# Performance work log

Hardware: AMD Instinct MI355X
Metric: run time of the kernel (lower is better)

Reference implementation:

```python
import jax, jax.numpy as jnp
import numpy as np
from jax import lax

V, E, T, F, K = 100000, 300, 50, 100, 3
B, S = 32, 512


def setup_inputs() -> dict:
    key = jax.random.key(0)
    ks = jax.random.split(key, 10)
    inp = {
        "x": jax.random.randint(ks[0], (B, S), 0, V),
        "tags": jax.random.randint(ks[1], (B, S), 0, T),
        "emb": jax.random.normal(ks[2], (V, E), dtype=jnp.float32),
        "conv_w": jax.random.normal(ks[3], (F, E, K), dtype=jnp.float32) / np.sqrt(E * K),
        "conv_b": jnp.zeros((F,), dtype=jnp.float32),
        "fc_w": jax.random.normal(ks[4], (T, F), dtype=jnp.float32) / np.sqrt(F),
        "fc_b": jnp.zeros((T,), dtype=jnp.float32),
        "start_trans": jax.random.uniform(ks[5], (T,), dtype=jnp.float32, minval=-0.1, maxval=0.1),
        "end_trans": jax.random.uniform(ks[6], (T,), dtype=jnp.float32, minval=-0.1, maxval=0.1),
        "trans": jax.random.uniform(ks[7], (T, T), dtype=jnp.float32, minval=-0.1, maxval=0.1),
    }
    return inp


def _emissions(x, emb, conv_w, conv_b, fc_w, fc_b):
    e = emb[x]                                   # [B,S,E] embedding gather
    e = jnp.transpose(e, (0, 2, 1))              # [B,E,S]
    h = lax.conv_general_dilated(e, conv_w, (1,), [(K // 2, K // 2)])  # [B,F,S] (NCW/OIW)
    h = jax.nn.relu(h + conv_b[None, :, None])   # dropout is identity in eval
    feat = jnp.transpose(h, (0, 2, 1))           # [B,S,F]
    return (jnp.einsum("bsf,tf->bst", feat, fc_w) + fc_b).astype(jnp.float32)  # [B,S,T]


def _crf_nll(emissions, tags, start_trans, end_trans, trans):
    # numerator: score of the gold tag path (full mask)
    em_tag = jnp.take_along_axis(emissions, tags[..., None], axis=-1)[..., 0]  # [B,S]
    num = (start_trans[tags[:, 0]]
           + em_tag.sum(-1)
           + trans[tags[:, :-1], tags[:, 1:]].sum(-1)
           + end_trans[tags[:, -1]])                                           # [B]

    # denominator: forward algorithm via scan over time
    alpha0 = start_trans[None, :] + emissions[:, 0]                             # [B,T]

    def step(alpha, em_t):
        # alpha: [B,T] prev scores; em_t: [B,T] emissions at t
        new = jax.nn.logsumexp(alpha[:, :, None] + trans[None] + em_t[:, None, :], axis=1)
        return new, None

    alpha, _ = lax.scan(step, alpha0, jnp.transpose(emissions[:, 1:], (1, 0, 2)))
    log_z = jax.nn.logsumexp(alpha + end_trans[None, :], axis=-1)               # [B]
    return -(num - log_z).sum()  # torchcrf default reduction='sum'; model returns -llh


def reference(x, tags, emb, conv_w, conv_b, fc_w, fc_b, start_trans, end_trans, trans):
    emissions = _emissions(x, emb, conv_w, conv_b, fc_w, fc_b)
    return _crf_nll(emissions, tags, start_trans, end_trans, trans)
```

## Files before the change

### kernel.cpp

```cpp
#include <hip/hip_runtime.h>
#include <hip/hip_bf16.h>
#include <math.h>

#define BB 32
#define SS 512
#define EE 300
#define FF 100
#define TT 50
#define CH 16
#define NC 32

typedef __attribute__((ext_vector_type(8))) short v8s;
typedef __attribute__((ext_vector_type(4))) float v4f;
#define MFMA16 __builtin_amdgcn_mfma_f32_16x16x32_bf16

#define AP 328
#define NCH 10
#define CKS 3
#define CHB (128 * 96)
#define A2P 152
#define MP 72

__device__ inline unsigned short f2bf(float v) {
    unsigned u = __float_as_uint(v);
    unsigned r = u + 0x7fff + ((u >> 16) & 1);
    return (unsigned short)(r >> 16);
}
__device__ inline float bf2f(short s) {
    return __uint_as_float(((unsigned)(unsigned short)s) << 16);
}
__device__ inline v8s ldsld8(const short* p) {
    return *(const v8s*)__builtin_assume_aligned(p, 16);
}
__device__ inline void g2lds16(const void* g, void* l) {
    __builtin_amdgcn_global_load_lds(
        (const __attribute__((address_space(1))) unsigned int*)g,
        (__attribute__((address_space(3))) unsigned int*)l, 16, 0, 0);
}

__global__ void prep_kernel(const float* __restrict__ tr, const float* __restrict__ cw,
                            const float* __restrict__ fcw,
                            unsigned short* __restrict__ wB2,
                            unsigned short* __restrict__ fcwT2,
                            unsigned short* __restrict__ AT,
                            unsigned short* __restrict__ Ab)
{
    const int gid = blockIdx.x * 256 + threadIdx.x;
    const int gs  = 64 * 256;
    for (int idx = gid; idx < NCH * CKS * 8 * 512; idx += gs) {
        int e = idx & 7, p = (idx >> 3) & 63, blk = idx >> 9;
        int ch = blk / 24, rem = blk - ch * 24;
        int sl = rem >> 3, ft = rem & 7;
        int col = p >> 2, q = p & 3;
        int n  = ft * 16 + col;
        int gk = ch * 96 + sl * 32 + q * 8 + e;
        int kk = gk / 320, ee = gk - kk * 320;
        float v = (n < FF && ee < EE) ? cw[n * 900 + ee * 3 + kk] : 0.f;
        wB2[idx] = f2bf(v);
    }
    for (int idx = gid; idx < 16 * 512; idx += gs) {
        int e = idx & 7, p = (idx >> 3) & 63, blk = idx >> 9;
        int ks = blk >> 2, nt = blk & 3;
        int col = p >> 2, q = p & 3;
        int t = nt * 16 + col, f = ks * 32 + q * 8 + e;
        float v = (t < TT && f < FF) ? fcw[t * FF + f] : 0.f;
        fcwT2[idx] = f2bf(v);
    }
    for (int idx = gid; idx < 64 * 64; idx += gs) {
        int r = idx >> 6, c2 = idx & 63;
        AT[idx] = (r < TT && c2 < TT) ? f2bf(__expf(tr[c2 * TT + r])) : 0;
        Ab[idx] = (r < TT && c2 < TT) ? f2bf(__expf(tr[r * TT + c2])) : 0;
    }
}

__global__ __launch_bounds__(256, 2) void emis_kernel(
    const int* __restrict__ x, const float* __restrict__ emb,
    const unsigned short* __restrict__ wB2, const float* __restrict__ cb,
    const unsigned short* __restrict__ fcwT2, const float* __restrict__ fcb,
    const int* __restrict__ tags,
    float* __restrict__ expem, float* __restrict__ rmv, float* __restrict__ emtag)
{
    __shared__ __align__(16) short ldsA[34 * AP];
    __shared__ __align__(16) short ldsB[2][CHB];

    const int b    = blockIdx.y;
    const int s0   = blockIdx.x * 32;
    const int tid  = threadIdx.x;
    const int wv   = tid >> 6;
    const int lane = tid & 63;
    const int col  = lane & 15;
    const int q    = lane >> 4;
    const int bofs = ((col << 2) | q) << 3;

#pragma unroll
    for (int it = 0; it < 6; ++it) {
        int seg = it * 4 + wv;
        g2lds16((const char*)wB2 + seg * 1024 + lane * 16,
                (char*)ldsB[0] + seg * 1024);
    }

    for (int g = tid; g < 34 * 75; g += 256) {
        int r = g / 75, eg = g - r * 75; int e0 = eg * 4;
        int gsq = s0 - 1 + r;
        short4 o;
        if (gsq >= 0 && gsq < SS) {
            int xr = x[b * SS + gsq];
            const float4 v = *(const float4*)(emb + (size_t)xr * EE + e0);
            o = make_short4((short)f2bf(v.x), (short)f2bf(v.y),
                            (short)f2bf(v.z), (short)f2bf(v.w));
        } else o = make_short4(0, 0, 0, 0);
        *(short4*)&ldsA[r * AP + e0] = o;
    }
    if (tid < 34 * 5) {
        int r = tid / 5, c0 = 300 + (tid % 5) * 4;
        *(short4*)&ldsA[r * AP + c0] = make_short4(0, 0, 0, 0);
    }
    __syncthreads();

    v4f acc[2][2];
#pragma unroll
    for (int a = 0; a < 2; ++a)
#pragma unroll
        for (int f = 0; f < 2; ++f) acc[a][f] = (v4f){0.f, 0.f, 0.f, 0.f};

    const int ftA = wv * 2, ftB = wv * 2 + 1;
    for (int ch = 0; ch < NCH; ++ch) {
        if (ch < NCH - 1) {
            const char* g = (const char*)(wB2 + (size_t)(ch + 1) * CHB);
            char* l = (char*)ldsB[(ch + 1) & 1];
#pragma unroll
            for (int it = 0; it < 6; ++it) {
                int seg = it * 4 + wv;
                g2lds16(g + seg * 1024 + lane * 16, l + seg * 1024);
            }
        }
        const short* Bc = ldsB[ch & 1];
#pragma unroll
        for (int sl = 0; sl < CKS; ++sl) {
            int gk = ch * 96 + sl * 32;
            int kk = (gk >= 640) ? 2 : (gk >= 320 ? 1 : 0);
            int e0 = gk - kk * 320;
            v8s a0 = ldsld8(&ldsA[(col + kk) * AP + e0 + q * 8]);
            v8s a1 = ldsld8(&ldsA[(16 + col + kk) * AP + e0 + q * 8]);
            v8s b0 = ldsld8(&Bc[((sl * 8 + ftA) << 9) + bofs]);
            v8s b1 = ldsld8(&Bc[((sl * 8 + ftB) << 9) + bofs]);
            acc[0][0] = MFMA16(a0, b0, acc[0][0], 0, 0, 0);
            acc[0][1] = MFMA16(a0, b1, acc[0][1], 0, 0, 0);
            acc[1][0] = MFMA16(a1, b0, acc[1][0], 0, 0, 0);
            acc[1][1] = MFMA16(a1, b1, acc[1][1], 0, 0, 0);
        }
        __syncthreads();
    }

    short* A2 = ldsB[0];
    short* B2 = ldsB[1];
#pragma unroll
    for (int it = 0; it < 4; ++it) {
        int seg = it * 4 + wv;
        g2lds16((const char*)fcwT2 + seg * 1024 + lane * 16,
                (char*)B2 + seg * 1024);
    }
#pragma unroll
    for (int st = 0; st < 2; ++st)
#pragma unroll
        for (int fi = 0; fi < 2; ++fi) {
            int f = (wv * 2 + fi) * 16 + col;
            float bias = (f < FF) ? cb[f] : 0.f;
#pragma unroll
            for (int rg = 0; rg < 4; ++rg) {
                int s = st * 16 + q * 4 + rg;
                float v = (f < FF) ? fmaxf(acc[st][fi][rg] + bias, 0.f) : 0.f;
                A2[s * A2P + f] = (short)f2bf(v);
            }
        }
    __syncthreads();

    if (wv < 2) {
        v4f a2[4];
#pragma unroll
        for (int nt = 0; nt < 4; ++nt) a2[nt] = (v4f){0.f, 0.f, 0.f, 0.f};
#pragma unroll
        for (int ks = 0; ks < 4; ++ks) {
            v8s af = ldsld8(&A2[(wv * 16 + col) * A2P + ks * 32 + q * 8]);
#pragma unroll
            for (int nt = 0; nt < 4; ++nt) {
                v8s bt = ldsld8(&B2[((ks * 4 + nt) << 9) + bofs]);
                a2[nt] = MFMA16(af, bt, a2[nt], 0, 0, 0);
            }
        }
        float fb0 = fcb[col], fb1 = fcb[16 + col], fb2 = fcb[32 + col];
        float fb3 = (col < 2) ? fcb[48 + col] : 0.f;
#pragma unroll
        for (int rg = 0; rg < 4; ++rg) {
            int s = s0 + wv * 16 + q * 4 + rg;
            float e0v = a2[0][rg] + fb0;
            float e1v = a2[1][rg] + fb1;
            float e2v = a2[2][rg] + fb2;
            float e3v = (col < 2) ? a2[3][rg] + fb3 : -1e30f;
            float m = fmaxf(fmaxf(e0v, e1v), fmaxf(e2v, e3v));
#pragma unroll
            for (int off = 1; off < 16; off <<= 1) m = fmaxf(m, __shfl_xor(m, off));
            int gidx = b * SS + s;
            if (col == 0) rmv[gidx] = m;
            int tg = tags[gidx];
            float* orow = expem + (size_t)gidx * TT;
            orow[col]      = __expf(e0v - m);
            orow[16 + col] = __expf(e1v - m);
            orow[32 + col] = __expf(e2v - m);
            if (col < 2) orow[48 + col] = __expf(e3v - m);
            if (tg == col)            emtag[gidx] = e0v;
            else if (tg == 16 + col)  emtag[gidx] = e1v;
            else if (tg == 32 + col)  emtag[gidx] = e2v;
            else if (col < 2 && tg == 48 + col) emtag[gidx] = e3v;
        }
    }
}

__global__ __launch_bounds__(64) void chunk_kernel(
    const float* __restrict__ expem, const unsigned short* __restrict__ AT,
    const unsigned short* __restrict__ Ab,
    unsigned short* __restrict__ R, float* __restrict__ lsR)
{
    __shared__ __align__(16) short L[2][64 * MP];
    __shared__ __align__(16) float emL[CH][64];
    const int c = blockIdx.x, b = blockIdx.y;
    const int lane = threadIdx.x;
    const int col = lane & 15, q = lane >> 4;
    const int t0 = c * CH + 1;
    const int nf = (c == NC - 1) ? (SS - 1 - (NC - 1) * CH) : CH;

    for (int idx = lane; idx < CH * 64; idx += 64) {
        int k = idx >> 6, m = idx & 63;
        float v = 0.f;
        if (m < TT && k < nf) v = expem[((size_t)(b * SS + t0 + k)) * TT + m];
        emL[k][m] = v;
    }

    v8s af[4][2];
#pragma unroll
    for (int jt = 0; jt < 4; ++jt)
#pragma unroll
        for (int kc = 0; kc < 2; ++kc)
            af[jt][kc] = *(const v8s*)(AT + (jt * 16 + col) * 64 + kc * 32 + q * 8);
    __syncthreads();

    {
        const v8s* arow = (const v8s*)(Ab + lane * 64);
#pragma unroll
        for (int g = 0; g < 8; ++g) {
            v8s a = arow[g];
            v8s o;
#pragma unroll
            for (int e = 0; e < 8; ++e)
                o[e] = (short)f2bf(bf2f(a[e]) * emL[0][g * 8 + e]);
            *(v8s*)&L[0][lane * MP + g * 8] = o;
        }
    }

    int cur = 0;
    for (int k = 1; k < nf; ++k) {
        __syncthreads();
        v8s bf[4][2];
#pragma unroll
        for (int nt = 0; nt < 4; ++nt)
#pragma unroll
            for (int kc = 0; kc < 2; ++kc)
                bf[nt][kc] = ldsld8(&L[cur][(nt * 16 + col) * MP + kc * 32 + q * 8]);
        v4f acc[4][4];
#pragma unroll
        for (int jt = 0; jt < 4; ++jt)
#pragma unroll
            for (int nt = 0; nt < 4; ++nt) {
                acc[jt][nt] = (v4f){0.f, 0.f, 0.f, 0.f};
                acc[jt][nt] = MFMA16(af[jt][0], bf[nt][0], acc[jt][nt], 0, 0, 0);
                acc[jt][nt] = MFMA16(af[jt][1], bf[nt][1], acc[jt][nt], 0, 0, 0);
            }
        if (k < nf - 1) {
#pragma unroll
            for (int jt = 0; jt < 4; ++jt) {
                const float4 em4 = *(const float4*)&emL[k][jt * 16 + q * 4];
#pragma unroll
                for (int nt = 0; nt < 4; ++nt) {
                    short4 o;
                    o.x = (short)f2bf(acc[jt][nt][0] * em4.x);
                    o.y = (short)f2bf(acc[jt][nt][1] * em4.y);
                    o.z = (short)f2bf(acc[jt][nt][2] * em4.z);
                    o.w = (short)f2bf(acc[jt][nt][3] * em4.w);
                    *(short4*)&L[cur ^ 1][(nt * 16 + col) * MP + jt * 16 + q * 4] = o;
                }
            }
            cur ^= 1;
        } else {
            float vals[4][4][4];
            float mx = 0.f;
#pragma unroll
            for (int jt = 0; jt < 4; ++jt) {
                const float4 em4 = *(const float4*)&emL[k][jt * 16 + q * 4];
#pragma unroll
                for (int nt = 0; nt < 4; ++nt) {
                    vals[jt][nt][0] = acc[jt][nt][0] * em4.x;
                    vals[jt][nt][1] = acc[jt][nt][1] * em4.y;
                    vals[jt][nt][2] = acc[jt][nt][2] * em4.z;
                    vals[jt][nt][3] = acc[jt][nt][3] * em4.w;
#pragma unroll
                    for (int r = 0; r < 4; ++r) mx = fmaxf(mx, vals[jt][nt][r]);
                }
            }
#pragma unroll
            for (int off = 1; off < 64; off <<= 1) mx = fmaxf(mx, __shfl_xor(mx, off));
            mx = fmaxf(mx, 1e-37f);
            float inv = 1.f / mx;
            unsigned short* Rc = R + ((size_t)(b * NC + c) << 12);
#pragma unroll
            for (int jt = 0; jt < 4; ++jt)
#pragma unroll
                for (int nt = 0; nt < 4; ++nt)
#pragma unroll
                    for (int r = 0; r < 4; ++r)
                        Rc[(jt * 16 + q * 4 + r) * 64 + nt * 16 + col] =
                            f2bf(vals[jt][nt][r] * inv);
            if (lane == 0) lsR[b * NC + c] = __logf(mx);
        }
    }
}

__global__ __launch_bounds__(256) void chain_kernel(
    const float* __restrict__ expem, const unsigned short* __restrict__ R,
    const float* __restrict__ lsR, const float* __restrict__ start,
    const float* __restrict__ endt,
    const float* __restrict__ emtag, const float* __restrict__ rmv,
    const int* __restrict__ tags, const float* __restrict__ tr,
    float* __restrict__ nllpart)
{
    __shared__ __align__(16) float pvec[64];
    __shared__ float red[8];
    __shared__ float lzsh;
    const int b = blockIdx.x, tid = threadIdx.x;
    const int wv = tid >> 6, i = tid & 63;

    if (wv == 0) {
        pvec[i] = (i < TT) ? __expf(start[i]) * expem[((size_t)(b * SS)) * TT + i] : 0.f;
        const unsigned short* Rb = R + ((size_t)(b * NC) << 12);
        v8s rb[3][8];
#pragma unroll
        for (int pc = 0; pc < 3; ++pc)
#pragma unroll
            for (int g = 0; g < 8; ++g)
                rb[pc][g] = *(const v8s*)(Rb + ((size_t)pc << 12) + i * 64 + g * 8);
        float logacc = 0.f;
#pragma unroll
        for (int c = 0; c < NC; ++c) {
            const int slot = c % 3;
            float acc = 0.f;
            const float4* pv = (const float4*)pvec;
#pragma unroll
            for (int g = 0; g < 8; ++g) {
                v8s v = rb[slot][g];
                float4 pA = pv[g * 2], pB = pv[g * 2 + 1];
                acc = fmaf(bf2f(v[0]), pA.x, acc);
                acc = fmaf(bf2f(v[1]), pA.y, acc);
                acc = fmaf(bf2f(v[2]), pA.z, acc);
                acc = fmaf(bf2f(v[3]), pA.w, acc);
                acc = fmaf(bf2f(v[4]), pB.x, acc);
                acc = fmaf(bf2f(v[5]), pB.y, acc);
                acc = fmaf(bf2f(v[6]), pB.z, acc);
                acc = fmaf(bf2f(v[7]), pB.w, acc);
            }
            if (c + 3 < NC) {
                const unsigned short* Rn = Rb + ((size_t)(c + 3) << 12);
#pragma unroll
                for (int g = 0; g < 8; ++g)
                    rb[slot][g] = *(const v8s*)(Rn + i * 64 + g * 8);
            }
            float mx = acc;
#pragma unroll
            for (int off = 1; off < 64; off <<= 1) mx = fmaxf(mx, __shfl_xor(mx, off));
            mx = fmaxf(mx, 1e-37f);
            logacc += __logf(mx) + lsR[b * NC + c];
            pvec[i] = acc * (1.f / mx);
        }
        float sv = (i < TT) ? pvec[i] * __expf(endt[i]) : 0.f;
#pragma unroll
        for (int off = 1; off < 64; off <<= 1) sv += __shfl_xor(sv, off);
        if (i == 0) lzsh = logacc + __logf(sv);
    } else {
        float accN = 0.f, accR = 0.f;
        for (int s = tid - 64; s < SS; s += 192) {
            int gi = b * SS + s;
            accN += emtag[gi];
            accR += rmv[gi];
            int tg = tags[gi];
            if (s < SS - 1) accN += tr[tg * TT + tags[gi + 1]];
        }
#pragma unroll
        for (int off = 1; off < 64; off <<= 1) {
            accN += __shfl_xor(accN, off);
            accR += __shfl_xor(accR, off);
        }
        if (i == 0) { red[wv] = accN; red[4 + wv] = accR; }
    }
    __syncthreads();
    if (tid == 0) {
        float tn  = red[1] + red[2] + red[3];
        float trm = red[5] + red[6] + red[7];
        float num = tn + start[tags[b * SS]] + endt[tags[b * SS + SS - 1]];
        nllpart[b] = trm + lzsh - num;
    }
}

__global__ void final_kernel(const float* __restrict__ nllpart, float* __restrict__ out)
{
    int tid = threadIdx.x;
    float v = (tid < BB) ? nllpart[tid] : 0.f;
#pragma unroll
    for (int off = 1; off < 64; off <<= 1) v += __shfl_xor(v, off);
    if (tid == 0) out[0] = v;
}

extern "C" void kernel_launch(void* const* d_in, const int* in_sizes, int n_in,
                              void* d_out, int out_size, void* d_ws, size_t ws_size,
                              hipStream_t stream)
{
    const int*   x    = (const int*)d_in[0];
    const int*   tags = (const int*)d_in[1];
    const float* emb  = (const float*)d_in[2];
    const float* cw   = (const float*)d_in[3];
    const float* cb   = (const float*)d_in[4];
    const float* fcw  = (const float*)d_in[5];
    const float* fcb  = (const float*)d_in[6];
    const float* st   = (const float*)d_in[7];
    const float* en   = (const float*)d_in[8];
    const float* tr   = (const float*)d_in[9];

    unsigned short* wB2   = (unsigned short*)d_ws;
    unsigned short* fcwT2 = wB2 + NCH * CKS * 8 * 512;
    unsigned short* ATm   = fcwT2 + 16 * 512;
    unsigned short* Abm   = ATm + 4096;
    unsigned short* Rm    = Abm + 4096;
    float* fbase   = (float*)(Rm + (size_t)BB * NC * 4096);
    float* expem   = fbase;
    float* rmv     = expem + (size_t)BB * SS * TT;
    float* emtag   = rmv + BB * SS;
    float* lsR     = emtag + BB * SS;
    float* nllpart = lsR + BB * NC;

    prep_kernel<<<dim3(64), 256, 0, stream>>>(tr, cw, fcw, wB2, fcwT2, ATm, Abm);
    emis_kernel<<<dim3(16, BB), 256, 0, stream>>>(x, emb, wB2, cb, fcwT2, fcb,
                                                  tags, expem, rmv, emtag);
    chunk_kernel<<<dim3(NC, BB), 64, 0, stream>>>(expem, ATm, Abm, Rm, lsR);
    chain_kernel<<<dim3(BB), 256, 0, stream>>>(expem, Rm, lsR, st, en,
                                               emtag, rmv, tags, tr, nllpart);
    final_kernel<<<dim3(1), 64, 0, stream>>>(nllpart, (float*)d_out);
}
```

Measured before the change: 249.8 us.

## Single-buffer conv weights, batch embedding gathers, pack bf16, fuse final reduction

The emission kernel drops the double-buffered weight LDS tile to a single buffer and raises the launch bound to three blocks per CU. It reuses ldsA for the FC stage, shrinks its pitch, and issues all embedding gathers up front so more loads are in flight. bf16 conversions use packed two-wide intrinsics. The final reduction kernel is removed: the chain kernel accumulates with atomics and the last block writes the output. The trade-off is that the next weight chunk load no longer overlaps compute, and the float atomic sum order becomes nondeterministic.

```diff
diff --git a/kernel.cpp b/kernel.cpp
--- a/kernel.cpp
+++ b/kernel.cpp
@@ -18,7 +18,7 @@
 #define NCH 10
 #define CKS 3
 #define CHB (128 * 96)
-#define A2P 152
+#define A2P 136
 #define MP 72
 
 __device__ inline unsigned short f2bf(float v) {
@@ -28,6 +28,10 @@
 }
 __device__ inline float bf2f(short s) {
     return __uint_as_float(((unsigned)(unsigned short)s) << 16);
+}
+__device__ inline unsigned pkbf2(float a, float b) {
+    __hip_bfloat162 h = __float22bfloat162_rn(make_float2(a, b));
+    return *(unsigned*)&h;
 }
 __device__ inline v8s ldsld8(const short* p) {
     return *(const v8s*)__builtin_assume_aligned(p, 16);
@@ -43,10 +47,12 @@
                             unsigned short* __restrict__ wB2,
                             unsigned short* __restrict__ fcwT2,
                             unsigned short* __restrict__ AT,
-                            unsigned short* __restrict__ Ab)
+                            unsigned short* __restrict__ Ab,
+                            float* __restrict__ accum, unsigned* __restrict__ cnt)
 {
     const int gid = blockIdx.x * 256 + threadIdx.x;
     const int gs  = 64 * 256;
+    if (gid == 0) { *accum = 0.f; *cnt = 0u; }
     for (int idx = gid; idx < NCH * CKS * 8 * 512; idx += gs) {
         int e = idx & 7, p = (idx >> 3) & 63, blk = idx >> 9;
         int ch = blk / 24, rem = blk - ch * 24;
@@ -73,7 +79,7 @@
     }
 }
 
-__global__ __launch_bounds__(256, 2) void emis_kernel(
+__global__ __launch_bounds__(256, 3) void emis_kernel(
     const int* __restrict__ x, const float* __restrict__ emb,
     const unsigned short* __restrict__ wB2, const float* __restrict__ cb,
     const unsigned short* __restrict__ fcwT2, const float* __restrict__ fcb,
@@ -81,7 +87,7 @@
     float* __restrict__ expem, float* __restrict__ rmv, float* __restrict__ emtag)
 {
     __shared__ __align__(16) short ldsA[34 * AP];
-    __shared__ __align__(16) short ldsB[2][CHB];
+    __shared__ __align__(16) short ldsB[CHB];
 
     const int b    = blockIdx.y;
     const int s0   = blockIdx.x * 32;
@@ -96,26 +102,40 @@
     for (int it = 0; it < 6; ++it) {
         int seg = it * 4 + wv;
         g2lds16((const char*)wB2 + seg * 1024 + lane * 16,
-                (char*)ldsB[0] + seg * 1024);
-    }
-
-    for (int g = tid; g < 34 * 75; g += 256) {
-        int r = g / 75, eg = g - r * 75; int e0 = eg * 4;
-        int gsq = s0 - 1 + r;
-        short4 o;
-        if (gsq >= 0 && gsq < SS) {
-            int xr = x[b * SS + gsq];
-            const float4 v = *(const float4*)(emb + (size_t)xr * EE + e0);
-            o = make_short4((short)f2bf(v.x), (short)f2bf(v.y),
-                            (short)f2bf(v.z), (short)f2bf(v.w));
-        } else o = make_short4(0, 0, 0, 0);
-        *(short4*)&ldsA[r * AP + e0] = o;
+                (char*)ldsB + seg * 1024);
+    }
+
+    int   xr[10], ofs[10], e0a[10];
+#pragma unroll
+    for (int it = 0; it < 10; ++it) {
+        int g = tid + it * 256;
+        int r = g / 75, eg = g - r * 75;
+        int e0 = eg * 4;
+        int src = s0 - 1 + r;
+        bool v = (g < 2550) && (src >= 0) && (src < SS);
+        xr[it]  = v ? x[b * SS + src] : -1;
+        ofs[it] = r * AP + e0;
+        e0a[it] = e0;
+    }
+    float4 vv[10];
+#pragma unroll
+    for (int it = 0; it < 10; ++it)
+        vv[it] = (xr[it] >= 0)
+               ? *(const float4*)(emb + (size_t)xr[it] * EE + e0a[it])
+               : make_float4(0.f, 0.f, 0.f, 0.f);
+#pragma unroll
+    for (int it = 0; it < 10; ++it) {
+        int g = tid + it * 256;
+        if (g < 2550) {
+            unsigned lo = pkbf2(vv[it].x, vv[it].y);
+            unsigned hi = pkbf2(vv[it].z, vv[it].w);
+            *(uint2*)&ldsA[ofs[it]] = make_uint2(lo, hi);
+        }
     }
     if (tid < 34 * 5) {
         int r = tid / 5, c0 = 300 + (tid % 5) * 4;
         *(short4*)&ldsA[r * AP + c0] = make_short4(0, 0, 0, 0);
     }
-    __syncthreads();
 
     v4f acc[2][2];
 #pragma unroll
@@ -125,16 +145,7 @@
 
     const int ftA = wv * 2, ftB = wv * 2 + 1;
     for (int ch = 0; ch < NCH; ++ch) {
-        if (ch < NCH - 1) {
-            const char* g = (const char*)(wB2 + (size_t)(ch + 1) * CHB);
-            char* l = (char*)ldsB[(ch + 1) & 1];
-#pragma unroll
-            for (int it = 0; it < 6; ++it) {
-                int seg = it * 4 + wv;
-                g2lds16(g + seg * 1024 + lane * 16, l + seg * 1024);
-            }
-        }
-        const short* Bc = ldsB[ch & 1];
+        __syncthreads();
 #pragma unroll
         for (int sl = 0; sl < CKS; ++sl) {
             int gk = ch * 96 + sl * 32;
@@ -142,18 +153,26 @@
             int e0 = gk - kk * 320;
             v8s a0 = ldsld8(&ldsA[(col + kk) * AP + e0 + q * 8]);
             v8s a1 = ldsld8(&ldsA[(16 + col + kk) * AP + e0 + q * 8]);
-            v8s b0 = ldsld8(&Bc[((sl * 8 + ftA) << 9) + bofs]);
-            v8s b1 = ldsld8(&Bc[((sl * 8 + ftB) << 9) + bofs]);
+            v8s b0 = ldsld8(&ldsB[((sl * 8 + ftA) << 9) + bofs]);
+            v8s b1 = ldsld8(&ldsB[((sl * 8 + ftB) << 9) + bofs]);
             acc[0][0] = MFMA16(a0, b0, acc[0][0], 0, 0, 0);
             acc[0][1] = MFMA16(a0, b1, acc[0][1], 0, 0, 0);
             acc[1][0] = MFMA16(a1, b0, acc[1][0], 0, 0, 0);
             acc[1][1] = MFMA16(a1, b1, acc[1][1], 0, 0, 0);
         }
         __syncthreads();
-    }
-
-    short* A2 = ldsB[0];
-    short* B2 = ldsB[1];
+        if (ch < NCH - 1) {
+            const char* g = (const char*)(wB2 + (size_t)(ch + 1) * CHB);
+#pragma unroll
+            for (int it = 0; it < 6; ++it) {
+                int seg = it * 4 + wv;
+                g2lds16(g + seg * 1024 + lane * 16, (char*)ldsB + seg * 1024);
+            }
+        }
+    }
+
+    short* A2 = ldsA;
+    short* B2 = ldsB;
 #pragma unroll
     for (int it = 0; it < 4; ++it) {
         int seg = it * 4 + wv;
@@ -249,11 +268,12 @@
 #pragma unroll
         for (int g = 0; g < 8; ++g) {
             v8s a = arow[g];
-            v8s o;
-#pragma unroll
-            for (int e = 0; e < 8; ++e)
-                o[e] = (short)f2bf(bf2f(a[e]) * emL[0][g * 8 + e]);
-            *(v8s*)&L[0][lane * MP + g * 8] = o;
+            float f[8];
+#pragma unroll
+            for (int e = 0; e < 8; ++e) f[e] = bf2f(a[e]) * emL[0][g * 8 + e];
+            uint4 o = make_uint4(pkbf2(f[0], f[1]), pkbf2(f[2], f[3]),
+                                 pkbf2(f[4], f[5]), pkbf2(f[6], f[7]));
+            *(uint4*)&L[0][lane * MP + g * 8] = o;
         }
     }
 
@@ -281,12 +301,10 @@
                 const float4 em4 = *(const float4*)&emL[k][jt * 16 + q * 4];
 #pragma unroll
                 for (int nt = 0; nt < 4; ++nt) {
-                    short4 o;
-                    o.x = (short)f2bf(acc[jt][nt][0] * em4.x);
-                    o.y = (short)f2bf(acc[jt][nt][1] * em4.y);
-                    o.z = (short)f2bf(acc[jt][nt][2] * em4.z);
-                    o.w = (short)f2bf(acc[jt][nt][3] * em4.w);
-                    *(short4*)&L[cur ^ 1][(nt * 16 + col) * MP + jt * 16 + q * 4] = o;
+                    uint2 o = make_uint2(
+                        pkbf2(acc[jt][nt][0] * em4.x, acc[jt][nt][1] * em4.y),
+                        pkbf2(acc[jt][nt][2] * em4.z, acc[jt][nt][3] * em4.w));
+                    *(uint2*)&L[cur ^ 1][(nt * 16 + col) * MP + jt * 16 + q * 4] = o;
                 }
             }
             cur ^= 1;
@@ -330,7 +348,8 @@
     const float* __restrict__ endt,
     const float* __restrict__ emtag, const float* __restrict__ rmv,
     const int* __restrict__ tags, const float* __restrict__ tr,
-    float* __restrict__ nllpart)
+    float* __restrict__ accum, unsigned* __restrict__ cnt,
+    float* __restrict__ out)
 {
     __shared__ __align__(16) float pvec[64];
     __shared__ float red[8];
@@ -404,17 +423,12 @@
         float tn  = red[1] + red[2] + red[3];
         float trm = red[5] + red[6] + red[7];
         float num = tn + start[tags[b * SS]] + endt[tags[b * SS + SS - 1]];
-        nllpart[b] = trm + lzsh - num;
-    }
-}
-
-__global__ void final_kernel(const float* __restrict__ nllpart, float* __restrict__ out)
-{
-    int tid = threadIdx.x;
-    float v = (tid < BB) ? nllpart[tid] : 0.f;
-#pragma unroll
-    for (int off = 1; off < 64; off <<= 1) v += __shfl_xor(v, off);
-    if (tid == 0) out[0] = v;
+        float nll = trm + lzsh - num;
+        atomicAdd(accum, nll);
+        __threadfence();
+        unsigned old = atomicAdd(cnt, 1u);
+        if (old == BB - 1) out[0] = atomicAdd(accum, 0.f);
+    }
 }
 
 extern "C" void kernel_launch(void* const* d_in, const int* in_sizes, int n_in,
@@ -442,13 +456,15 @@
     float* rmv     = expem + (size_t)BB * SS * TT;
     float* emtag   = rmv + BB * SS;
     float* lsR     = emtag + BB * SS;
-    float* nllpart = lsR + BB * NC;
-
-    prep_kernel<<<dim3(64), 256, 0, stream>>>(tr, cw, fcw, wB2, fcwT2, ATm, Abm);
+    float* accum   = lsR + BB * NC;
+    unsigned* cnt  = (unsigned*)(accum + 1);
+
+    prep_kernel<<<dim3(64), 256, 0, stream>>>(tr, cw, fcw, wB2, fcwT2, ATm, Abm,
+                                              accum, cnt);
     emis_kernel<<<dim3(16, BB), 256, 0, stream>>>(x, emb, wB2, cb, fcwT2, fcb,
                                                   tags, expem, rmv, emtag);
     chunk_kernel<<<dim3(NC, BB), 64, 0, stream>>>(expem, ATm, Abm, Rm, lsR);
     chain_kernel<<<dim3(BB), 256, 0, stream>>>(expem, Rm, lsR, st, en,
-                                               emtag, rmv, tags, tr, nllpart);
-    final_kernel<<<dim3(1), 64, 0, stream>>>(nllpart, (float*)d_out);
-}
+                                               emtag, rmv, tags, tr,
+                                               accum, cnt, (float*)d_out);
+}
```

Result: faster. 241.1 us (-3.5%).
